# Optimization experiments

Hardware: AMD Instinct MI355X
Metric: run time of the kernel (lower is better)

## Reference

```python
import jax, jax.numpy as jnp
import numpy as np

B, L, H, E, M = 8, 1024, 1024, 2048, 2048  # batch, seq, hidden_dim, expanded_dim, max_seq_length


def setup_inputs() -> dict:
    key = jax.random.key(0)
    ks = jax.random.split(key, 10)
    n = lambda k, shape, s=0.02: jax.random.normal(k, shape, jnp.float32) * s
    return {
        'x': jax.random.normal(ks[0], (B, L, H), jnp.float32),
        'ln1_w': jnp.ones((H,), jnp.float32), 'ln1_b': jnp.zeros((H,), jnp.float32),
        'ln2_w': jnp.ones((E,), jnp.float32), 'ln2_b': jnp.zeros((E,), jnp.float32),
        'w_qkv': n(ks[1], (3 * E, H)), 'b_qkv': jnp.zeros((3 * E,), jnp.float32),
        'w_out': n(ks[2], (H, E)), 'b_out': jnp.zeros((H,), jnp.float32),
        'rel_pos': n(ks[3], (2 * M - 1, H)),
        'w_beta': n(ks[4], (E, 2 * H)), 'b_beta': jnp.zeros((E,), jnp.float32),
        'w1': n(ks[5], (4 * H, H)), 'b1': jnp.zeros((4 * H,), jnp.float32),
        'w2': n(ks[6], (H, 4 * H)), 'b2': jnp.zeros((H,), jnp.float32),
        'conv_w': n(ks[7], (E, 1, 3), 0.3),  # depthwise conv1d weight [C,1,K]
        'attn_scale': jnp.ones((1,), jnp.float32),
    }


def _ln(x, w, b):
    m = jnp.mean(x, -1, keepdims=True)
    v = jnp.mean((x - m) ** 2, -1, keepdims=True)
    return (x - m) / jnp.sqrt(v + 1e-5) * w + b


def _normalize(x):
    # F.normalize(x, dim=-1): x / max(||x||_2, 1e-12)
    return x / jnp.maximum(jnp.linalg.norm(x, axis=-1, keepdims=True), 1e-12)


def _dwconv(z, w):
    # z: [B,L,E]; depthwise conv1d k=3, pad=1, no bias (groups=E)
    y = jax.lax.conv_general_dilated(
        z.transpose(0, 2, 1), w, window_strides=(1,), padding=((1, 1),),
        feature_group_count=w.shape[0], dimension_numbers=('NCH', 'OIH', 'NCH'))
    return y.transpose(0, 2, 1)


def reference(x, ln1_w, ln1_b, ln2_w, ln2_b, w_qkv, b_qkv, w_out, b_out,
              rel_pos, w_beta, b_beta, w1, b1, w2, b2, conv_w, attn_scale):
    Lx = x.shape[1]
    h = _ln(x, ln1_w, ln1_b)
    qkv = h @ w_qkv.T + b_qkv
    q, k, v = jnp.split(qkv, 3, axis=-1)  # each [B,L,E]
    q = jax.nn.silu(q)
    k = jax.nn.silu(k)
    v = jax.nn.gelu(v, approximate=False)
    # interdependent normalize-mix (k uses the updated q)
    q = _normalize(q) + 0.1 * k
    k = _normalize(k) + 0.1 * q
    q = _dwconv(q, conv_w)
    k = _dwconv(k, conv_w)
    v = _dwconv(v, conv_w)
    # position-conditioned beta gate
    pos_embed = rel_pos[:Lx]  # [L,H]
    pos_info = jnp.einsum('blh,mh->blm', h, pos_embed).mean(-1, keepdims=True)  # [B,L,1]
    comb = jnp.concatenate([h, jnp.broadcast_to(pos_info, h.shape)], axis=-1)  # [B,L,2H]
    beta = jax.nn.sigmoid(comb @ w_beta.T + b_beta) * 0.9 + 0.1  # [B,L,E]
    # delta-rule: state starts at zeros so v_old = state @ k^T = 0 exactly
    v_new = beta * v  # beta*v + (1-beta)*0
    state = jnp.einsum('ble,blf->bef', v_new, k)  # v_new^T @ k : [B,E,E]
    out = jnp.einsum('ble,bfe->blf', q, state) * attn_scale  # q @ state^T
    out = _ln(out, ln2_w, ln2_b) @ w_out.T + b_out
    x = x + out
    h2 = _ln(x, ln1_w, ln1_b)  # norm1 is reused pre-MLP
    mlp = jax.nn.gelu(h2 @ w1.T + b1, approximate=False) @ w2.T + b2
    return x + mlp
```

## Files before the change

kernel.cpp:

```cpp
#include <hip/hip_runtime.h>
#include <hip/hip_bf16.h>
#include <math.h>

using bf16 = __hip_bfloat16;
typedef __attribute__((ext_vector_type(8))) short bf16x8;
typedef __attribute__((ext_vector_type(4))) float f32x4;

#define DEVI __device__ __forceinline__

DEVI float b2f(bf16 v) { return __bfloat162float(v); }
DEVI bf16 f2b(float v) { return __float2bfloat16(v); }
DEVI short b2s(bf16 v) { return *reinterpret_cast<short*>(&v); }
DEVI float s2f(short s) {
  unsigned int u = ((unsigned int)(unsigned short)s) << 16;
  return __uint_as_float(u);
}
DEVI float geluf(float x) { return 0.5f * x * (1.0f + erff(x * 0.70710678118654752f)); }
DEVI float siluf(float x) { return x / (1.0f + expf(-x)); }
DEVI float fsilu(float x) { return x / (1.0f + __expf(-x)); }

DEVI void load_lds16(const bf16* g, bf16* l) {
  __builtin_amdgcn_global_load_lds(
      (const __attribute__((address_space(1))) void*)g,
      (__attribute__((address_space(3))) void*)l, 16, 0, 0);
}

__global__ __launch_bounds__(256) void cast_kernel(const float* __restrict__ in,
                                                   bf16* __restrict__ out, int n4) {
  int i = blockIdx.x * 256 + threadIdx.x;
  if (i >= n4) return;
  float4 v = reinterpret_cast<const float4*>(in)[i];
  bf16 o[4] = { f2b(v.x), f2b(v.y), f2b(v.z), f2b(v.w) };
  reinterpret_cast<uint2*>(out)[i] = *reinterpret_cast<uint2*>(o);
}

__global__ __launch_bounds__(256) void prep_kernel(const float* __restrict__ rel,
                                                   float* __restrict__ pm,
                                                   const float* __restrict__ wb,
                                                   float* __restrict__ wb2s) {
  const int b = blockIdx.x;
  if (b < 4) {
    int h = b * 256 + threadIdx.x;
    float s = 0.f;
    for (int m = 0; m < 1024; ++m) s += rel[m * 1024 + h];
    pm[h] = s * (1.0f / 1024.0f);
  } else {
    int e = (b - 4) * 4 + (threadIdx.x >> 6);
    int lane = threadIdx.x & 63;
    float s = 0.f;
    for (int j = lane; j < 1024; j += 64) s += wb[(long)e * 2048 + 1024 + j];
#pragma unroll
    for (int off = 32; off > 0; off >>= 1) s += __shfl_down(s, off);
    if (lane == 0) wb2s[e] = s;
  }
}

__global__ __launch_bounds__(256) void convw_pack_kernel(const float* __restrict__ cw,
                                                         bf16* __restrict__ wpl) {
  int e = blockIdx.x * 256 + threadIdx.x;
  wpl[e]        = f2b(cw[e * 3]);
  wpl[2048 + e] = f2b(cw[e * 3 + 1]);
  wpl[4096 + e] = f2b(cw[e * 3 + 2]);
}

template<bool POS>
__global__ __launch_bounds__(256) void ln1024_kernel(
    const float* __restrict__ x, const float* __restrict__ w, const float* __restrict__ b,
    bf16* __restrict__ out, const float* __restrict__ pmean, float* __restrict__ pos) {
  __shared__ float red[12];
  long row = blockIdx.x;
  int t = threadIdx.x, lane = t & 63, wid = t >> 6;
  float4 xv = reinterpret_cast<const float4*>(x + row * 1024)[t];
  float s = xv.x + xv.y + xv.z + xv.w;
  float ss = xv.x * xv.x + xv.y * xv.y + xv.z * xv.z + xv.w * xv.w;
#pragma unroll
  for (int off = 32; off > 0; off >>= 1) { s += __shfl_down(s, off); ss += __shfl_down(ss, off); }
  if (lane == 0) { red[wid] = s; red[4 + wid] = ss; }
  __syncthreads();
  s = red[0] + red[1] + red[2] + red[3];
  ss = red[4] + red[5] + red[6] + red[7];
  float mean = s * (1.0f / 1024.0f);
  float rstd = rsqrtf(ss * (1.0f / 1024.0f) - mean * mean + 1e-5f);
  float4 wv = reinterpret_cast<const float4*>(w)[t];
  float4 bv = reinterpret_cast<const float4*>(b)[t];
  float h0 = (xv.x - mean) * rstd * wv.x + bv.x;
  float h1 = (xv.y - mean) * rstd * wv.y + bv.y;
  float h2 = (xv.z - mean) * rstd * wv.z + bv.z;
  float h3 = (xv.w - mean) * rstd * wv.w + bv.w;
  bf16 o[4] = { f2b(h0), f2b(h1), f2b(h2), f2b(h3) };
  reinterpret_cast<uint2*>(out + row * 1024)[t] = *reinterpret_cast<uint2*>(o);
  if (POS) {
    float4 pv = reinterpret_cast<const float4*>(pmean)[t];
    float d = h0 * pv.x + h1 * pv.y + h2 * pv.z + h3 * pv.w;
#pragma unroll
    for (int off = 32; off > 0; off >>= 1) d += __shfl_down(d, off);
    if (lane == 0) red[8 + wid] = d;
    __syncthreads();
    if (t == 0) pos[row] = red[8] + red[9] + red[10] + red[11];
  }
}

__global__ __launch_bounds__(256) void ln1024b_kernel(
    const bf16* __restrict__ x, const float* __restrict__ w, const float* __restrict__ b,
    bf16* __restrict__ out) {
  __shared__ float red[8];
  long row = blockIdx.x;
  int t = threadIdx.x, lane = t & 63, wid = t >> 6;
  bf16 tv[4];
  *reinterpret_cast<uint2*>(tv) = reinterpret_cast<const uint2*>(x + row * 1024)[t];
  float v[4], s = 0.f, ss = 0.f;
#pragma unroll
  for (int j = 0; j < 4; ++j) { v[j] = b2f(tv[j]); s += v[j]; ss += v[j] * v[j]; }
#pragma unroll
  for (int off = 32; off > 0; off >>= 1) { s += __shfl_down(s, off); ss += __shfl_down(ss, off); }
  if (lane == 0) { red[wid] = s; red[4 + wid] = ss; }
  __syncthreads();
  s = red[0] + red[1] + red[2] + red[3];
  ss = red[4] + red[5] + red[6] + red[7];
  float mean = s * (1.0f / 1024.0f);
  float rstd = rsqrtf(ss * (1.0f / 1024.0f) - mean * mean + 1e-5f);
  float4 wv = reinterpret_cast<const float4*>(w)[t];
  float4 bv = reinterpret_cast<const float4*>(b)[t];
  bf16 o[4];
  o[0] = f2b((v[0] - mean) * rstd * wv.x + bv.x);
  o[1] = f2b((v[1] - mean) * rstd * wv.y + bv.y);
  o[2] = f2b((v[2] - mean) * rstd * wv.z + bv.z);
  o[3] = f2b((v[3] - mean) * rstd * wv.w + bv.w);
  reinterpret_cast<uint2*>(out + row * 1024)[t] = *reinterpret_cast<uint2*>(o);
}

__global__ __launch_bounds__(256) void ln2048_bf16_kernel(
    const bf16* __restrict__ in, const float* __restrict__ w, const float* __restrict__ b,
    bf16* __restrict__ out) {
  __shared__ float red[8];
  long row = blockIdx.x;
  int t = threadIdx.x, lane = t & 63, wid = t >> 6;
  bf16 tv[8];
  *reinterpret_cast<int4*>(tv) = reinterpret_cast<const int4*>(in + row * 2048)[t];
  float v[8], s = 0.f, ss = 0.f;
#pragma unroll
  for (int j = 0; j < 8; ++j) { v[j] = b2f(tv[j]); s += v[j]; ss += v[j] * v[j]; }
#pragma unroll
  for (int off = 32; off > 0; off >>= 1) { s += __shfl_down(s, off); ss += __shfl_down(ss, off); }
  if (lane == 0) { red[wid] = s; red[4 + wid] = ss; }
  __syncthreads();
  s = red[0] + red[1] + red[2] + red[3];
  ss = red[4] + red[5] + red[6] + red[7];
  float mean = s * (1.0f / 2048.0f);
  float rstd = rsqrtf(ss * (1.0f / 2048.0f) - mean * mean + 1e-5f);
  int base = t * 8;
  bf16 o[8];
#pragma unroll
  for (int j = 0; j < 8; ++j) o[j] = f2b((v[j] - mean) * rstd * w[base + j] + b[base + j]);
  reinterpret_cast<int4*>(out + row * 2048)[t] = *reinterpret_cast<int4*>(o);
}

#define QK_TAP(RR, WV) { \
  float qmv = s2f(qs[RR][j]), kmv = s2f(ks[RR][j]); \
  float qn = qmv * rq[RR] + 0.1f * kmv; \
  float kn = kmv * rk[RR] + 0.1f * qn; \
  accq += b2f(WV[j]) * b2f(f2b(qn)); \
  acck += b2f(WV[j]) * b2f(f2b(kn)); }

__global__ __launch_bounds__(256) void actconv_qk_kernel(
    const bf16* __restrict__ qraw, const bf16* __restrict__ kraw,
    bf16* __restrict__ qout, bf16* __restrict__ kout, const bf16* __restrict__ wpl) {
  __shared__ float red[10][2][4];
  const int t = threadIdx.x, lane = t & 63, wid = t >> 6;
  const int e0 = t * 8;
  const int bb = blockIdx.x >> 7;
  const int l0 = (blockIdx.x & 127) * 8;
  const long rowbase = (long)bb * 1024 * 2048;
  bf16x8 qs[10], ks[10];
#pragma unroll
  for (int r = 0; r < 10; ++r) {
    int dl = l0 + r - 1;
    float sq = 0.f, sk = 0.f;
    if (dl >= 0 && dl < 1024) {
      long off = rowbase + (long)dl * 2048 + e0;
      bf16 tq[8], tk[8];
      *reinterpret_cast<int4*>(tq) = *reinterpret_cast<const int4*>(qraw + off);
      *reinterpret_cast<int4*>(tk) = *reinterpret_cast<const int4*>(kraw + off);
#pragma unroll
      for (int j = 0; j < 8; ++j) {
        float qv = fsilu(b2f(tq[j])); sq += qv * qv; qs[r][j] = b2s(f2b(qv));
        float kv = fsilu(b2f(tk[j])); sk += kv * kv; ks[r][j] = b2s(f2b(kv));
      }
    } else {
      qs[r] = 0; ks[r] = 0;
    }
#pragma unroll
    for (int off = 32; off > 0; off >>= 1) { sq += __shfl_down(sq, off); sk += __shfl_down(sk, off); }
    if (lane == 0) { red[r][0][wid] = sq; red[r][1][wid] = sk; }
  }
  __syncthreads();
  float rq[10], rk[10];
#pragma unroll
  for (int r = 0; r < 10; ++r) {
    float sq = red[r][0][0] + red[r][0][1] + red[r][0][2] + red[r][0][3];
    float sk = red[r][1][0] + red[r][1][1] + red[r][1][2] + red[r][1][3];
    rq[r] = 1.0f / fmaxf(sqrtf(sq), 1e-12f);
    rk[r] = 1.0f / fmaxf(sqrtf(sk), 1e-12f);
  }
  bf16 w0[8], w1[8], w2[8];
  *reinterpret_cast<int4*>(w0) = *reinterpret_cast<const int4*>(wpl + e0);
  *reinterpret_cast<int4*>(w1) = *reinterpret_cast<const int4*>(wpl + 2048 + e0);
  *reinterpret_cast<int4*>(w2) = *reinterpret_cast<const int4*>(wpl + 4096 + e0);
#pragma unroll
  for (int rr = 1; rr <= 8; ++rr) {
    const int l = l0 + rr - 1;
    bf16 oq[8], ok[8];
#pragma unroll
    for (int j = 0; j < 8; ++j) {
      float accq = 0.f, acck = 0.f;
      QK_TAP(rr, w1);
      if (l > 0)    QK_TAP(rr - 1, w0);
      if (l < 1023) QK_TAP(rr + 1, w2);
      oq[j] = f2b(accq); ok[j] = f2b(acck);
    }
    long off = rowbase + (long)l * 2048 + e0;
    *reinterpret_cast<int4*>(qout + off) = *reinterpret_cast<int4*>(oq);
    *reinterpret_cast<int4*>(kout + off) = *reinterpret_cast<int4*>(ok);
  }
}

__global__ __launch_bounds__(256) void transpose_vb_kernel(
    const bf16* __restrict__ vraw, const bf16* __restrict__ beta,
    bf16* __restrict__ vt, const bf16* __restrict__ wpl) {
  const long base = (long)blockIdx.z * 2097152;
  const int r0 = blockIdx.y * 64 + ((threadIdx.x & 63) >> 3) * 8;
  const int c0 = blockIdx.x * 256 + (threadIdx.x >> 6) * 64 + (threadIdx.x & 7) * 8;
  bf16 g[10][8];
#pragma unroll
  for (int j = 0; j < 10; ++j) {
    int r = r0 + j - 1;
    if (r >= 0 && r < 1024) {
      bf16 raw[8];
      *reinterpret_cast<int4*>(raw) =
          *reinterpret_cast<const int4*>(&vraw[base + (long)r * 2048 + c0]);
#pragma unroll
      for (int i = 0; i < 8; ++i) g[j][i] = f2b(geluf(b2f(raw[i])));
    } else {
#pragma unroll
      for (int i = 0; i < 8; ++i) g[j][i] = f2b(0.f);
    }
  }
  bf16 w0[8], w1[8], w2[8];
  *reinterpret_cast<int4*>(w0) = *reinterpret_cast<const int4*>(&wpl[c0]);
  *reinterpret_cast<int4*>(w1) = *reinterpret_cast<const int4*>(&wpl[2048 + c0]);
  *reinterpret_cast<int4*>(w2) = *reinterpret_cast<const int4*>(&wpl[4096 + c0]);
  bf16 vv[8][8];
#pragma unroll
  for (int j = 0; j < 8; ++j) {
    const int l = r0 + j;
    bf16 bt[8];
    *reinterpret_cast<int4*>(bt) =
        *reinterpret_cast<const int4*>(&beta[base + (long)l * 2048 + c0]);
#pragma unroll
    for (int i = 0; i < 8; ++i) {
      float a = b2f(w1[i]) * b2f(g[j + 1][i]);
      if (l > 0)    a += b2f(w0[i]) * b2f(g[j][i]);
      if (l < 1023) a += b2f(w2[i]) * b2f(g[j + 2][i]);
      vv[j][i] = f2b(b2f(bt[i]) * a);
    }
  }
#pragma unroll
  for (int i = 0; i < 8; ++i) {
    bf16 w[8];
#pragma unroll
    for (int j = 0; j < 8; ++j) w[j] = vv[j][i];
    *reinterpret_cast<int4*>(&vt[base + (long)(c0 + i) * 1024 + r0]) =
        *reinterpret_cast<int4*>(w);
  }
}

enum { EPI_QKV = 0, EPI_BETA = 1, EPI_BF16 = 2, EPI_SCALE = 3, EPI_RES_F32 = 4, EPI_GELU = 5 };

#define MF(d, a, b) d = __builtin_amdgcn_mfma_f32_16x16x32_bf16(a, b, d, 0, 0, 0)
#define RD_A(S, MR, KK) \
  (*reinterpret_cast<const bf16x8*>(&smem[(S)*16384 + wm*8192 + ((MR)*16 + r16)*64 + ((((KK)*32) + kq8) ^ swz)]))
#define RD_B(S, NR, KK) \
  (*reinterpret_cast<const bf16x8*>(&smem[32768 + (S)*16384 + (wn>>1)*8192 + ((wn&1)*64 + (NR)*16 + r16)*64 + ((((KK)*32) + kq8) ^ swz)]))
#define STAGE_A1(S, H, Q, KT) \
  load_lds16(Abase + (long)((H)*128 + (Q)*64) * lda + (long)(KT)*64, \
             &smem[(S)*16384 + (H)*8192 + (Q)*4096 + wid*512])
#define STAGE_B1(S, H, Q, KT) \
  load_lds16(Bbase + (long)((H)*128 + (Q)*64) * ldb + (long)(KT)*64, \
             &smem[32768 + (S)*16384 + (H)*8192 + (Q)*4096 + wid*512])
#define STAGE_AH(S, H, KT) { STAGE_A1(S, H, 0, KT); STAGE_A1(S, H, 1, KT); }
#define STAGE_BH(S, H, KT) { STAGE_B1(S, H, 0, KT); STAGE_B1(S, H, 1, KT); }
#define BAR_A __builtin_amdgcn_s_barrier()
#define LGKM0 { asm volatile("s_waitcnt lgkmcnt(0)" ::: "memory"); __builtin_amdgcn_sched_barrier(0); }
#define VWAIT(LST) { if (LST) { asm volatile("s_waitcnt vmcnt(0)" ::: "memory"); } \
                     else     { asm volatile("s_waitcnt vmcnt(6)" ::: "memory"); } \
                     __builtin_amdgcn_sched_barrier(0); }

#define KTILE(S, ST1, ST2, ST3, ST4, W4) { \
  bf16x8 aL[4][2], aH[4][2], bL[2][2], bH[2][2]; \
  _Pragma("unroll") for (int m_ = 0; m_ < 4; ++m_) { aL[m_][0] = RD_A(S, m_, 0); aL[m_][1] = RD_A(S, m_, 1); } \
  _Pragma("unroll") for (int n_ = 0; n_ < 2; ++n_) { bL[n_][0] = RD_B(S, n_, 0); bL[n_][1] = RD_B(S, n_, 1); } \
  ST1; BAR_A; LGKM0; \
  __builtin_amdgcn_s_setprio(1); \
  _Pragma("unroll") for (int m_ = 0; m_ < 4; ++m_) _Pragma("unroll") for (int n_ = 0; n_ < 2; ++n_) { \
    MF(acc[m_][n_], aL[m_][0], bL[n_][0]); MF(acc[m_][n_], aL[m_][1], bL[n_][1]); } \
  __builtin_amdgcn_s_setprio(0); __builtin_amdgcn_s_barrier(); \
  _Pragma("unroll") for (int n_ = 0; n_ < 2; ++n_) { bH[n_][0] = RD_B(S, n_ + 2, 0); bH[n_][1] = RD_B(S, n_ + 2, 1); } \
  ST2; BAR_A; LGKM0; \
  __builtin_amdgcn_s_setprio(1); \
  _Pragma("unroll") for (int m_ = 0; m_ < 4; ++m_) _Pragma("unroll") for (int n_ = 0; n_ < 2; ++n_) { \
    MF(acc[m_][n_ + 2], aL[m_][0], bH[n_][0]); MF(acc[m_][n_ + 2], aL[m_][1], bH[n_][1]); } \
  __builtin_amdgcn_s_setprio(0); __builtin_amdgcn_s_barrier(); \
  _Pragma("unroll") for (int m_ = 0; m_ < 4; ++m_) { aH[m_][0] = RD_A(S, m_ + 4, 0); aH[m_][1] = RD_A(S, m_ + 4, 1); } \
  ST3; BAR_A; LGKM0; \
  __builtin_amdgcn_s_setprio(1); \
  _Pragma("unroll") for (int m_ = 0; m_ < 4; ++m_) _Pragma("unroll") for (int n_ = 0; n_ < 2; ++n_) { \
    MF(acc[m_ + 4][n_], aH[m_][0], bL[n_][0]); MF(acc[m_ + 4][n_], aH[m_][1], bL[n_][1]); } \
  __builtin_amdgcn_s_setprio(0); __builtin_amdgcn_s_barrier(); \
  ST4; W4; BAR_A; LGKM0; \
  __builtin_amdgcn_s_setprio(1); \
  _Pragma("unroll") for (int m_ = 0; m_ < 4; ++m_) _Pragma("unroll") for (int n_ = 0; n_ < 2; ++n_) { \
    MF(acc[m_ + 4][n_ + 2], aH[m_][0], bH[n_][0]); MF(acc[m_ + 4][n_ + 2], aH[m_][1], bH[n_][1]); } \
  __builtin_amdgcn_s_setprio(0); __builtin_amdgcn_s_barrier(); \
}

template<int EPI>
__global__ __launch_bounds__(512) void gemm256_kernel(
    const bf16* __restrict__ A, int lda, long sA,
    const bf16* __restrict__ B, int ldb, long sB,
    void* __restrict__ Cv, int ldc, long sC, int K,
    const float* __restrict__ bias, const float* __restrict__ aux_row,
    const float* __restrict__ aux_col, const bf16* __restrict__ vconv,
    const float* __restrict__ resid, const float* __restrict__ scale_ptr,
    bf16* __restrict__ p2, bf16* __restrict__ p3) {
  __shared__ bf16 smem[65536];
  const int bz = blockIdx.z;
  A += (long)bz * sA;
  B += (long)bz * sB;
  const int m0 = blockIdx.y * 256, n0 = blockIdx.x * 256;
  const int t = threadIdx.x, lane = t & 63, wid = t >> 6;
  const int wm = wid >> 2, wn = wid & 3;
  const int r16 = lane & 15, kq8 = (lane >> 4) * 8;
  const int swz = (r16 & 7) << 3;
  const int lrow = lane >> 3;
  const int cswz = ((lane & 7) ^ lrow) * 8;
  const bf16* Abase = A + (long)(m0 + wid * 8 + lrow) * lda + cswz;
  const bf16* Bbase = B + (long)(n0 + wid * 8 + lrow) * ldb + cswz;
  f32x4 acc[8][4] = {};
  const int NT = K >> 6, NIT = NT >> 1;
  STAGE_AH(0, 0, 0); STAGE_AH(0, 1, 0); STAGE_BH(0, 0, 0); STAGE_BH(0, 1, 0);
  STAGE_BH(1, 0, 1); STAGE_BH(1, 1, 1); STAGE_AH(1, 0, 1);
  asm volatile("s_waitcnt vmcnt(6)" ::: "memory");
  __builtin_amdgcn_sched_barrier(0);
  __builtin_amdgcn_s_barrier();
  for (int i = 0; i < NIT; ++i) {
    const int tb = 2 * i;
    const bool lst = (i == NIT - 1);
    KTILE(0,
      { STAGE_AH(1, 1, tb + 1); },
      { },
      { if (!lst) { STAGE_BH(0, 0, tb + 2); STAGE_BH(0, 1, tb + 2); } },
      { if (!lst) { STAGE_AH(0, 0, tb + 2); } },
      VWAIT(lst));
    KTILE(1,
      { if (!lst) { STAGE_AH(0, 1, tb + 2); } },
      { },
      { if (!lst) { STAGE_BH(1, 0, tb + 3); STAGE_BH(1, 1, tb + 3); } },
      { if (!lst) { STAGE_AH(1, 0, tb + 3); } },
      VWAIT(lst));
  }
  float scl = 1.0f;
  if (EPI == EPI_SCALE) scl = scale_ptr[0];
  const int rb = (lane >> 4) * 4;
#pragma unroll
  for (int mr = 0; mr < 8; ++mr) {
#pragma unroll
    for (int nr = 0; nr < 4; ++nr) {
#pragma unroll
      for (int r = 0; r < 4; ++r) {
        const long gm = m0 + wm * 128 + mr * 16 + rb + r;
        const int gn = n0 + wn * 64 + nr * 16 + r16;
        const long idx = (long)bz * sC + gm * (long)ldc + gn;
        float v = acc[mr][nr][r];
        if (EPI == EPI_QKV) {
          const int seg = gn >> 11, cc = gn & 2047;
          bf16* dst = (seg == 0) ? (bf16*)Cv : (seg == 1) ? p2 : p3;
          dst[gm * 2048 + cc] = f2b(v + bias[gn]);
        } else if (EPI == EPI_BETA) {
          float tt = v + bias[gn] + aux_row[gm] * aux_col[gn];
          float be = 0.9f / (1.0f + expf(-tt)) + 0.1f;
          ((bf16*)Cv)[idx] = f2b(be);
        } else if (EPI == EPI_BF16) {
          ((bf16*)Cv)[idx] = f2b(v);
        } else if (EPI == EPI_SCALE) {
          ((bf16*)Cv)[idx] = f2b(v * scl);
        } else if (EPI == EPI_RES_F32) {
          ((float*)Cv)[idx] = v + bias[gn] + resid[idx];
        } else {
          ((bf16*)Cv)[idx] = f2b(geluf(v + bias[gn]));
        }
      }
    }
  }
}

#define A_RD(S, MR, KK) \
  (*reinterpret_cast<const bf16x8*>(&amem[(S)*8192 + (wm*64 + (MR)*16 + r16)*64 + ((((KK)*32) + kq8) ^ swz)]))
#define B_RD(S, NR, KK) \
  (*reinterpret_cast<const bf16x8*>(&amem[16384 + (S)*16384 + (wn*64 + (NR)*16 + r16)*64 + ((((KK)*32) + kq8) ^ swz)]))
#define A_ST(S, Q, KT) \
  load_lds16(Abase + (long)((Q)*64) * lda + (long)(KT)*64, &amem[(S)*8192 + (Q)*4096 + wid*512])
#define B_ST(S, Q, KT) \
  load_lds16(Bbase + (long)((Q)*64) * ldb + (long)(KT)*64, &amem[16384 + (S)*16384 + (Q)*4096 + wid*512])
#define STAGE_T(S, KT) { A_ST(S, 0, KT); A_ST(S, 1, KT); B_ST(S, 0, KT); B_ST(S, 1, KT); B_ST(S, 2, KT); B_ST(S, 3, KT); }

template<int RB, int WB, int NR>
__global__ __launch_bounds__(512) void gemmA128_kernel(
    const bf16* __restrict__ A, int lda, long sA,
    const bf16* __restrict__ B, int ldb, long sB,
    void* __restrict__ Cv, int ldc, long sC, int K,
    const float* __restrict__ bias, const void* __restrict__ residv) {
  __shared__ bf16 amem[49152];
  A += (long)blockIdx.z * sA;
  B += (long)blockIdx.z * sB;
  const int m0 = blockIdx.y * 128, n0 = blockIdx.x * 256;
  const int t = threadIdx.x, lane = t & 63, wid = t >> 6;
  const int wm = wid >> 2, wn = wid & 3;
  const int r16 = lane & 15, kq8 = (lane >> 4) * 8;
  const int swz = (r16 & 7) << 3;
  const int lrow = lane >> 3;
  const int cswz = ((lane & 7) ^ lrow) * 8;
  const bf16* Abase = A + (long)(m0 + wid * 8 + lrow) * lda + cswz;
  const bf16* Bbase = B + (long)(n0 + wid * 8 + lrow) * ldb + cswz;
  f32x4 acc[4][4] = {};
  const int NT = K >> 6;
  STAGE_T(0, 0); STAGE_T(1, 1);
  asm volatile("s_waitcnt vmcnt(6)" ::: "memory");
  __builtin_amdgcn_sched_barrier(0);
  __builtin_amdgcn_s_barrier();
  for (int tt = 0; tt < NT; ++tt) {
    const int S = tt & 1;
    const bool pre = (tt + 2 < NT);
    bf16x8 a[4][2], bL[2][2], bH[2][2];
#pragma unroll
    for (int m_ = 0; m_ < 4; ++m_) { a[m_][0] = A_RD(S, m_, 0); a[m_][1] = A_RD(S, m_, 1); }
#pragma unroll
    for (int n_ = 0; n_ < 2; ++n_) { bL[n_][0] = B_RD(S, n_, 0); bL[n_][1] = B_RD(S, n_, 1); }
#pragma unroll
    for (int n_ = 0; n_ < 2; ++n_) { bH[n_][0] = B_RD(S, n_ + 2, 0); bH[n_][1] = B_RD(S, n_ + 2, 1); }
    LGKM0;
    __builtin_amdgcn_s_setprio(1);
#pragma unroll
    for (int m_ = 0; m_ < 4; ++m_)
#pragma unroll
      for (int n_ = 0; n_ < 2; ++n_) {
        MF(acc[m_][n_], a[m_][0], bL[n_][0]); MF(acc[m_][n_], a[m_][1], bL[n_][1]);
      }
    __builtin_amdgcn_s_setprio(0);
    __builtin_amdgcn_s_barrier();
    __builtin_amdgcn_sched_barrier(0);
    if (pre) STAGE_T(S, tt + 2);
    __builtin_amdgcn_s_setprio(1);
#pragma unroll
    for (int m_ = 0; m_ < 4; ++m_)
#pragma unroll
      for (int n_ = 0; n_ < 2; ++n_) {
        MF(acc[m_][n_ + 2], a[m_][0], bH[n_][0]); MF(acc[m_][n_ + 2], a[m_][1], bH[n_][1]);
      }
    __builtin_amdgcn_s_setprio(0);
    if (pre) { asm volatile("s_waitcnt vmcnt(6)" ::: "memory"); }
    else     { asm volatile("s_waitcnt vmcnt(0)" ::: "memory"); }
    __builtin_amdgcn_sched_barrier(0);
    __builtin_amdgcn_s_barrier();
    __builtin_amdgcn_sched_barrier(0);
  }
  const int rb = (lane >> 4) * 4;
#pragma unroll
  for (int mr = 0; mr < 4; ++mr) {
#pragma unroll
    for (int nr = 0; nr < 4; ++nr) {
#pragma unroll
      for (int r = 0; r < 4; ++r) {
        const long gm = m0 + wm * 64 + mr * 16 + rb + r;
        const int gn = n0 + wn * 64 + nr * 16 + r16;
        const long idx = (long)blockIdx.z * sC + gm * (long)ldc + gn;
        float o = acc[mr][nr][r];
        if (!NR) {
          o += bias[gn];
          o += RB ? b2f(((const bf16*)residv)[idx]) : ((const float*)residv)[idx];
        }
        if (WB) ((bf16*)Cv)[idx] = f2b(o);
        else    ((float*)Cv)[idx] = o;
      }
    }
  }
}

extern "C" void kernel_launch(void* const* d_in, const int* in_sizes, int n_in,
                              void* d_out, int out_size, void* d_ws, size_t ws_size,
                              hipStream_t stream) {
  (void)in_sizes; (void)n_in; (void)out_size;
  const float* x       = (const float*)d_in[0];
  const float* ln1_w   = (const float*)d_in[1];
  const float* ln1_b   = (const float*)d_in[2];
  const float* ln2_w   = (const float*)d_in[3];
  const float* ln2_b   = (const float*)d_in[4];
  const float* w_qkv   = (const float*)d_in[5];
  const float* b_qkv   = (const float*)d_in[6];
  const float* w_out   = (const float*)d_in[7];
  const float* b_out   = (const float*)d_in[8];
  const float* rel_pos = (const float*)d_in[9];
  const float* w_beta  = (const float*)d_in[10];
  const float* b_beta  = (const float*)d_in[11];
  const float* w1      = (const float*)d_in[12];
  const float* b1      = (const float*)d_in[13];
  const float* w2      = (const float*)d_in[14];
  const float* b2      = (const float*)d_in[15];
  const float* conv_w  = (const float*)d_in[16];
  const float* attn_sc = (const float*)d_in[17];
  float* out = (float*)d_out;

  if (ws_size < 180400128UL) return;
  char* ws = (char*)d_ws;
  bf16*  wbuf    = (bf16*)(ws + 0);
  bf16*  wpl     = (bf16*)(ws + 11534336UL);
  float* pmean   = (float*)(ws + 12582912UL);
  float* wb2s    = (float*)(ws + 12587008UL);
  float* posinfo = (float*)(ws + 12595200UL);
  bf16* R0 = (bf16*)(ws + 12627968UL);
  bf16* R1 = (bf16*)(ws + 46182400UL);
  bf16* R2 = (bf16*)(ws + 79736832UL);
  bf16* R3 = (bf16*)(ws + 113291264UL);
  bf16* R4 = (bf16*)(ws + 146845696UL);
  bf16* vscr = (bf16*)d_out;
  bf16* x2b = R1;

  prep_kernel<<<516, 256, 0, stream>>>(rel_pos, pmean, w_beta, wb2s);

  ln1024_kernel<true><<<8192, 256, 0, stream>>>(x, ln1_w, ln1_b, R0, pmean, posinfo);

  cast_kernel<<<6144, 256, 0, stream>>>(w_qkv, wbuf, 1572864);
  gemm256_kernel<EPI_QKV><<<dim3(24, 32, 1), 512, 0, stream>>>(
      R0, 1024, 0, wbuf, 1024, 0, R1, 2048, 0, 1024,
      b_qkv, nullptr, nullptr, nullptr, nullptr, nullptr, R2, vscr);

  convw_pack_kernel<<<8, 256, 0, stream>>>(conv_w, wpl);

  actconv_qk_kernel<<<1024, 256, 0, stream>>>(R1, R2, R4, R3, wpl);

  cast_kernel<<<4096, 256, 0, stream>>>(w_beta, wbuf, 1048576);
  gemm256_kernel<EPI_BETA><<<dim3(8, 32, 1), 512, 0, stream>>>(
      R0, 1024, 0, wbuf, 2048, 0, R1, 2048, 0, 1024,
      b_beta, posinfo, wb2s, nullptr, nullptr, nullptr, nullptr, nullptr);

  transpose_vb_kernel<<<dim3(8, 16, 8), 256, 0, stream>>>(vscr, R1, R0, wpl);

  gemmA128_kernel<0, 1, 1><<<dim3(4, 8, 8), 512, 0, stream>>>(
      R4, 2048, 2097152, R3, 2048, 2097152, R2, 1024, 1048576, 2048,
      nullptr, nullptr);

  gemm256_kernel<EPI_SCALE><<<dim3(8, 4, 8), 512, 0, stream>>>(
      R2, 1024, 1048576, R0, 1024, 2097152, R3, 2048, 2097152, 1024,
      nullptr, nullptr, nullptr, nullptr, nullptr, attn_sc, nullptr, nullptr);

  ln2048_bf16_kernel<<<8192, 256, 0, stream>>>(R3, ln2_w, ln2_b, R0);

  cast_kernel<<<2048, 256, 0, stream>>>(w_out, wbuf, 524288);
  gemmA128_kernel<0, 1, 0><<<dim3(4, 64, 1), 512, 0, stream>>>(
      R0, 2048, 0, wbuf, 2048, 0, x2b, 1024, 0, 2048, b_out, x);

  ln1024b_kernel<<<8192, 256, 0, stream>>>(x2b, ln1_w, ln1_b, R2);

  cast_kernel<<<4096, 256, 0, stream>>>(w1, wbuf, 1048576);
  gemm256_kernel<EPI_GELU><<<dim3(16, 32, 1), 512, 0, stream>>>(
      R2, 1024, 0, wbuf, 1024, 0, R3, 4096, 0, 1024,
      b1, nullptr, nullptr, nullptr, nullptr, nullptr, nullptr, nullptr);

  cast_kernel<<<4096, 256, 0, stream>>>(w2, wbuf, 1048576);
  gemmA128_kernel<1, 0, 0><<<dim3(4, 64, 1), 512, 0, stream>>>(
      R3, 4096, 0, wbuf, 4096, 0, out, 1024, 0, 4096, b2, x2b);
}
```

Before: 643.3 us.

## Fuse QKV and beta GEMMs into one launch, merge weight casts and conv pack

Concatenates the w_qkv weights and the first half of w_beta into a single bf16 buffer, so one GEMM with 32 column tiles computes q, k, v and the sigmoid beta gate in one shared epilogue. The separate beta GEMM launch is gone, along with its rereading of the LN1 activations, and the grid becomes larger and more even. The two weight-cast kernels merge into one, and the conv-weight packing moves into prep_kernel, which cuts launches. Buffers are reassigned: beta now goes to R3 and transpose_vb runs before actconv, which adds risk of buffer aliasing errors.

```diff
diff --git a/kernel.cpp b/kernel.cpp
--- a/kernel.cpp
+++ b/kernel.cpp
@@ -16,7 +16,6 @@
   return __uint_as_float(u);
 }
 DEVI float geluf(float x) { return 0.5f * x * (1.0f + erff(x * 0.70710678118654752f)); }
-DEVI float siluf(float x) { return x / (1.0f + expf(-x)); }
 DEVI float fsilu(float x) { return x / (1.0f + __expf(-x)); }
 
 DEVI void load_lds16(const bf16* g, bf16* l) {
@@ -34,17 +33,37 @@
   reinterpret_cast<uint2*>(out)[i] = *reinterpret_cast<uint2*>(o);
 }
 
+__global__ __launch_bounds__(256) void castqb_kernel(const float* __restrict__ wq,
+                                                     const float* __restrict__ wb,
+                                                     bf16* __restrict__ out) {
+  long g = (long)blockIdx.x * 256 + threadIdx.x;
+  if (g < 1572864) {
+    float4 v = reinterpret_cast<const float4*>(wq)[g];
+    bf16 o[4] = { f2b(v.x), f2b(v.y), f2b(v.z), f2b(v.w) };
+    reinterpret_cast<uint2*>(out)[g] = *reinterpret_cast<uint2*>(o);
+  } else {
+    long gb = g - 1572864;
+    long eb = gb >> 8;
+    long jb = (gb & 255) * 4;
+    float4 v = *reinterpret_cast<const float4*>(&wb[eb * 2048 + jb]);
+    bf16 o[4] = { f2b(v.x), f2b(v.y), f2b(v.z), f2b(v.w) };
+    *reinterpret_cast<uint2*>(&out[6291456 + eb * 1024 + jb]) = *reinterpret_cast<uint2*>(o);
+  }
+}
+
 __global__ __launch_bounds__(256) void prep_kernel(const float* __restrict__ rel,
                                                    float* __restrict__ pm,
                                                    const float* __restrict__ wb,
-                                                   float* __restrict__ wb2s) {
+                                                   float* __restrict__ wb2s,
+                                                   const float* __restrict__ cw,
+                                                   bf16* __restrict__ wpl) {
   const int b = blockIdx.x;
   if (b < 4) {
     int h = b * 256 + threadIdx.x;
     float s = 0.f;
     for (int m = 0; m < 1024; ++m) s += rel[m * 1024 + h];
     pm[h] = s * (1.0f / 1024.0f);
-  } else {
+  } else if (b < 516) {
     int e = (b - 4) * 4 + (threadIdx.x >> 6);
     int lane = threadIdx.x & 63;
     float s = 0.f;
@@ -52,15 +71,12 @@
 #pragma unroll
     for (int off = 32; off > 0; off >>= 1) s += __shfl_down(s, off);
     if (lane == 0) wb2s[e] = s;
-  }
-}
-
-__global__ __launch_bounds__(256) void convw_pack_kernel(const float* __restrict__ cw,
-                                                         bf16* __restrict__ wpl) {
-  int e = blockIdx.x * 256 + threadIdx.x;
-  wpl[e]        = f2b(cw[e * 3]);
-  wpl[2048 + e] = f2b(cw[e * 3 + 1]);
-  wpl[4096 + e] = f2b(cw[e * 3 + 2]);
+  } else {
+    int e = (b - 516) * 256 + threadIdx.x;
+    wpl[e]        = f2b(cw[e * 3]);
+    wpl[2048 + e] = f2b(cw[e * 3 + 1]);
+    wpl[4096 + e] = f2b(cw[e * 3 + 2]);
+  }
 }
 
 template<bool POS>
@@ -274,7 +290,7 @@
   }
 }
 
-enum { EPI_QKV = 0, EPI_BETA = 1, EPI_BF16 = 2, EPI_SCALE = 3, EPI_RES_F32 = 4, EPI_GELU = 5 };
+enum { EPI_QKVB = 0, EPI_SCALE = 1, EPI_GELU = 2 };
 
 #define MF(d, a, b) d = __builtin_amdgcn_mfma_f32_16x16x32_bf16(a, b, d, 0, 0, 0)
 #define RD_A(S, MR, KK) \
@@ -329,9 +345,9 @@
     const bf16* __restrict__ B, int ldb, long sB,
     void* __restrict__ Cv, int ldc, long sC, int K,
     const float* __restrict__ bias, const float* __restrict__ aux_row,
-    const float* __restrict__ aux_col, const bf16* __restrict__ vconv,
-    const float* __restrict__ resid, const float* __restrict__ scale_ptr,
-    bf16* __restrict__ p2, bf16* __restrict__ p3) {
+    const float* __restrict__ aux_col, const float* __restrict__ bias2,
+    const float* __restrict__ scale_ptr,
+    bf16* __restrict__ p2, bf16* __restrict__ p3, bf16* __restrict__ p4) {
   __shared__ bf16 smem[65536];
   const int bz = blockIdx.z;
   A += (long)bz * sA;
@@ -381,20 +397,18 @@
         const int gn = n0 + wn * 64 + nr * 16 + r16;
         const long idx = (long)bz * sC + gm * (long)ldc + gn;
         float v = acc[mr][nr][r];
-        if (EPI == EPI_QKV) {
+        if (EPI == EPI_QKVB) {
           const int seg = gn >> 11, cc = gn & 2047;
-          bf16* dst = (seg == 0) ? (bf16*)Cv : (seg == 1) ? p2 : p3;
-          dst[gm * 2048 + cc] = f2b(v + bias[gn]);
-        } else if (EPI == EPI_BETA) {
-          float tt = v + bias[gn] + aux_row[gm] * aux_col[gn];
-          float be = 0.9f / (1.0f + expf(-tt)) + 0.1f;
-          ((bf16*)Cv)[idx] = f2b(be);
-        } else if (EPI == EPI_BF16) {
-          ((bf16*)Cv)[idx] = f2b(v);
+          if (seg < 3) {
+            bf16* dst = (seg == 0) ? (bf16*)Cv : (seg == 1) ? p2 : p3;
+            dst[gm * 2048 + cc] = f2b(v + bias[gn]);
+          } else {
+            float tt = v + bias2[cc] + aux_row[gm] * aux_col[cc];
+            float be = 0.9f / (1.0f + expf(-tt)) + 0.1f;
+            p4[gm * 2048 + cc] = f2b(be);
+          }
         } else if (EPI == EPI_SCALE) {
           ((bf16*)Cv)[idx] = f2b(v * scl);
-        } else if (EPI == EPI_RES_F32) {
-          ((float*)Cv)[idx] = v + bias[gn] + resid[idx];
         } else {
           ((bf16*)Cv)[idx] = f2b(geluf(v + bias[gn]));
         }
@@ -534,25 +548,19 @@
   bf16* vscr = (bf16*)d_out;
   bf16* x2b = R1;
 
-  prep_kernel<<<516, 256, 0, stream>>>(rel_pos, pmean, w_beta, wb2s);
+  prep_kernel<<<524, 256, 0, stream>>>(rel_pos, pmean, w_beta, wb2s, conv_w, wpl);
 
   ln1024_kernel<true><<<8192, 256, 0, stream>>>(x, ln1_w, ln1_b, R0, pmean, posinfo);
 
-  cast_kernel<<<6144, 256, 0, stream>>>(w_qkv, wbuf, 1572864);
-  gemm256_kernel<EPI_QKV><<<dim3(24, 32, 1), 512, 0, stream>>>(
-      R0, 1024, 0, wbuf, 1024, 0, R1, 2048, 0, 1024,
-      b_qkv, nullptr, nullptr, nullptr, nullptr, nullptr, R2, vscr);
-
-  convw_pack_kernel<<<8, 256, 0, stream>>>(conv_w, wpl);
+  castqb_kernel<<<8192, 256, 0, stream>>>(w_qkv, w_beta, R4);
+
+  gemm256_kernel<EPI_QKVB><<<dim3(32, 32, 1), 512, 0, stream>>>(
+      R0, 1024, 0, R4, 1024, 0, R1, 2048, 0, 1024,
+      b_qkv, posinfo, wb2s, b_beta, nullptr, R2, vscr, R3);
+
+  transpose_vb_kernel<<<dim3(8, 16, 8), 256, 0, stream>>>(vscr, R3, R0, wpl);
 
   actconv_qk_kernel<<<1024, 256, 0, stream>>>(R1, R2, R4, R3, wpl);
-
-  cast_kernel<<<4096, 256, 0, stream>>>(w_beta, wbuf, 1048576);
-  gemm256_kernel<EPI_BETA><<<dim3(8, 32, 1), 512, 0, stream>>>(
-      R0, 1024, 0, wbuf, 2048, 0, R1, 2048, 0, 1024,
-      b_beta, posinfo, wb2s, nullptr, nullptr, nullptr, nullptr, nullptr);
-
-  transpose_vb_kernel<<<dim3(8, 16, 8), 256, 0, stream>>>(vscr, R1, R0, wpl);
 
   gemmA128_kernel<0, 1, 1><<<dim3(4, 8, 8), 512, 0, stream>>>(
       R4, 2048, 2097152, R3, 2048, 2097152, R2, 1024, 1048576, 2048,
@@ -560,7 +568,7 @@
 
   gemm256_kernel<EPI_SCALE><<<dim3(8, 4, 8), 512, 0, stream>>>(
       R2, 1024, 1048576, R0, 1024, 2097152, R3, 2048, 2097152, 1024,
-      nullptr, nullptr, nullptr, nullptr, nullptr, attn_sc, nullptr, nullptr);
+      nullptr, nullptr, nullptr, nullptr, attn_sc, nullptr, nullptr, nullptr);
 
   ln2048_bf16_kernel<<<8192, 256, 0, stream>>>(R3, ln2_w, ln2_b, R0);
 
```

Measured after the change: 720.9 us. 1.12x slower.
